# Kernel tuning notes

Hardware: AMD Instinct MI355X
Metric: run time of the kernel (lower is better)

Reference implementation:

```python
import jax, jax.numpy as jnp
import numpy as np

B, S, H, F, E, K = 4, 2048, 1024, 3584, 8, 2


def setup_inputs() -> dict:
    key = jax.random.key(0)
    ks = jax.random.split(key, 5)
    sc = 0.02
    return {
        "hidden_states": jax.random.normal(ks[0], (B, S, H), jnp.float32),
        "router_w": jax.random.normal(ks[1], (E, H), jnp.float32) * sc,
        "w1": jax.random.normal(ks[2], (E, F, H), jnp.float32) * sc,
        "v1": jax.random.normal(ks[3], (E, F, H), jnp.float32) * sc,
        "w2": jax.random.normal(ks[4], (E, F, H), jnp.float32) * sc,
    }


def reference(hidden_states, router_w, w1, v1, w2):
    b, s, h = hidden_states.shape
    x = hidden_states.reshape(-1, h)  # [T, H] tokens (transpose(0,1) is a no-op per-token)
    T = x.shape[0]
    n_exp = w1.shape[0]

    # --- Mixtral router: fp32 softmax, top-k, renormalize ---
    logits = x @ router_w.T  # [T, E]
    scores = jax.nn.softmax(logits.astype(jnp.float32), axis=-1)
    expert_weights, expert_indices = jax.lax.top_k(scores, K)  # [T, K]
    expert_weights = expert_weights / expert_weights.sum(axis=-1, keepdims=True)
    expert_weights = expert_weights.astype(x.dtype)

    # combine coefficients: coef[t, e] = sum_k weight[t,k] * (idx[t,k]==e)
    coef = jnp.zeros((T, n_exp), x.dtype)
    coef = coef.at[jnp.arange(T)[:, None], expert_indices].add(expert_weights)

    out = jnp.zeros_like(x)
    for e in range(n_exp):  # small fixed expert count
        hmid = jax.nn.silu(x @ w1[e].T) * (x @ v1[e].T)  # [T, F]
        out = out + coef[:, e:e + 1] * (hmid @ w2[e])  # [T, H]
    return out.reshape(b, s, h)
```

## Files before the change

### kernel.cpp

```cpp
#include <hip/hip_runtime.h>
#include <cstdint>
#include <cstddef>

#define T_TOK 8192
#define H_DIM 1024
#define F_DIM 3584
#define E_NUM 8
#define MAX_ROWS 17408
#define MAX_TILES 136

typedef __bf16 bf16_t;
typedef bf16_t bf16x8 __attribute__((ext_vector_type(8)));
typedef bf16_t bf16x4 __attribute__((ext_vector_type(4)));
typedef float floatx4 __attribute__((ext_vector_type(4)));

typedef const __attribute__((address_space(1))) void* gas_ptr;
typedef __attribute__((address_space(3))) void* las_ptr;

__device__ __forceinline__ void async_copy16(const void* g, void* l) {
    __builtin_amdgcn_global_load_lds((gas_ptr)g, (las_ptr)l, 16, 0, 0);
}

__global__ void cast_f32_to_bf16(const float* __restrict__ in, bf16_t* __restrict__ out, int n4) {
    int i = blockIdx.x * blockDim.x + threadIdx.x;
    if (i < n4) {
        const float4 v = ((const float4*)in)[i];
        bf16x4 o;
        o[0] = (bf16_t)v.x; o[1] = (bf16_t)v.y; o[2] = (bf16_t)v.z; o[3] = (bf16_t)v.w;
        ((bf16x4*)out)[i] = o;
    }
}

__global__ void transpose_cast_w2(const float* __restrict__ W2, bf16_t* __restrict__ W2T) {
    __shared__ bf16_t tile[32][34];
    const int e = blockIdx.z;
    const int f0 = blockIdx.x * 32;
    const int h0 = blockIdx.y * 32;
    const float* src = W2 + (size_t)e * F_DIM * H_DIM;
    bf16_t* dst = W2T + (size_t)e * H_DIM * F_DIM;
    const int tx = threadIdx.x;
    const int ty = threadIdx.y;
#pragma unroll
    for (int r = 0; r < 32; r += 8)
        tile[ty + r][tx] = (bf16_t)src[(size_t)(f0 + ty + r) * H_DIM + (h0 + tx)];
    __syncthreads();
#pragma unroll
    for (int r = 0; r < 32; r += 8)
        dst[(size_t)(h0 + ty + r) * F_DIM + (f0 + tx)] = tile[tx][ty + r];
}

__global__ void router_kernel(const float* __restrict__ X, const float* __restrict__ RW,
                              int* __restrict__ tok_e, float* __restrict__ tok_w) {
    const int lane = threadIdx.x & 63;
    const int wave = threadIdx.x >> 6;
    const int t = blockIdx.x * 4 + wave;
    const float* xp = X + (size_t)t * H_DIM;
    float xr[16];
#pragma unroll
    for (int j = 0; j < 16; ++j) xr[j] = xp[j * 64 + lane];
    float logits[E_NUM];
#pragma unroll
    for (int e = 0; e < E_NUM; ++e) {
        const float* rp = RW + e * H_DIM;
        float a = 0.f;
#pragma unroll
        for (int j = 0; j < 16; ++j) a += xr[j] * rp[j * 64 + lane];
#pragma unroll
        for (int s = 32; s; s >>= 1) a += __shfl_xor(a, s, 64);
        logits[e] = a;
    }
    if (lane == 0) {
        float mx = logits[0];
#pragma unroll
        for (int e = 1; e < E_NUM; ++e) mx = fmaxf(mx, logits[e]);
        float p[E_NUM], sum = 0.f;
#pragma unroll
        for (int e = 0; e < E_NUM; ++e) { p[e] = __expf(logits[e] - mx); sum += p[e]; }
#pragma unroll
        for (int e = 0; e < E_NUM; ++e) p[e] /= sum;
        int i0 = 0;
#pragma unroll
        for (int e = 1; e < E_NUM; ++e) if (p[e] > p[i0]) i0 = e;
        int i1 = (i0 == 0) ? 1 : 0;
#pragma unroll
        for (int e = 0; e < E_NUM; ++e) if (e != i0 && p[e] > p[i1]) i1 = e;
        const float s2 = p[i0] + p[i1];
        tok_e[t * 2 + 0] = i0; tok_w[t * 2 + 0] = p[i0] / s2;
        tok_e[t * 2 + 1] = i1; tok_w[t * 2 + 1] = p[i1] / s2;
    }
}

__global__ void build_assignments(const int* __restrict__ tok_e, const float* __restrict__ tok_w,
                                  int* __restrict__ asg_tok, float* __restrict__ asg_wt,
                                  int* __restrict__ tok_slot, int* __restrict__ tile_meta,
                                  int* __restrict__ n_tiles_out) {
    __shared__ int cnt[E_NUM];
    __shared__ int seg_start[E_NUM];
    __shared__ int seg_pad[E_NUM];
    const int tid = threadIdx.x;
    if (tid < E_NUM) cnt[tid] = 0;
    __syncthreads();
    for (int i = tid; i < T_TOK * 2; i += 1024) atomicAdd(&cnt[tok_e[i]], 1);
    __syncthreads();
    if (tid == 0) {
        int run = 0, nt = 0;
        for (int e = 0; e < E_NUM; ++e) {
            seg_start[e] = run;
            const int tiles = (cnt[e] + 127) >> 7;
            seg_pad[e] = tiles << 7;
            for (int j = 0; j < tiles; ++j) {
                tile_meta[nt * 2] = e;
                tile_meta[nt * 2 + 1] = run + j * 128;
                ++nt;
            }
            run += tiles << 7;
        }
        *n_tiles_out = nt;
    }
    __syncthreads();
    if (tid < E_NUM) cnt[tid] = 0;
    __syncthreads();
    for (int i = tid; i < T_TOK * 2; i += 1024) {
        const int e = tok_e[i];
        const int slot = atomicAdd(&cnt[e], 1);
        const int g = seg_start[e] + slot;
        asg_tok[g] = i >> 1;
        asg_wt[g] = tok_w[i];
        tok_slot[i] = g;
    }
    __syncthreads();
    for (int e = 0; e < E_NUM; ++e)
        for (int j = cnt[e] + tid; j < seg_pad[e]; j += 1024) {
            asg_tok[seg_start[e] + j] = -1;
            asg_wt[seg_start[e] + j] = 0.f;
        }
}


__global__ __launch_bounds__(256, 2)
void gemm1_glu(const bf16_t* __restrict__ X, const bf16_t* __restrict__ W1all,
               const bf16_t* __restrict__ V1all, const int* __restrict__ asg_tok,
               const float* __restrict__ asg_wt, const int* __restrict__ tile_meta,
               const int* __restrict__ n_tiles, bf16_t* __restrict__ Hmid) {
    const int tile = blockIdx.x;
    if (tile >= *n_tiles) return;
    const int e = tile_meta[tile * 2];
    const int row0 = tile_meta[tile * 2 + 1];
    const bf16_t* W1 = W1all + (size_t)e * F_DIM * H_DIM;
    const bf16_t* V1 = V1all + (size_t)e * F_DIM * H_DIM;

    __shared__ __attribute__((aligned(16))) bf16_t As[128 * 32];
    __shared__ __attribute__((aligned(16))) bf16_t B1s[128 * 32];
    __shared__ __attribute__((aligned(16))) bf16_t B2s[128 * 32];
    const int tid = threadIdx.x;
    const int lane = tid & 63;
    const int wave = tid >> 6;
    const int n0 = blockIdx.y * 128;
    const int wm = (wave >> 1) * 64;
    const int wn = (wave & 1) * 64;
    const int fr = lane & 15;
    const int q = lane >> 4;

    floatx4 acc1[4][4], acc2[4][4];
    const floatx4 zero = {0.f, 0.f, 0.f, 0.f};
#pragma unroll
    for (int a = 0; a < 4; ++a)
#pragma unroll
        for (int b = 0; b < 4; ++b) { acc1[a][b] = zero; acc2[a][b] = zero; }

    const int srow = tid >> 2;
    const int c = ((tid & 3) - ((tid >> 3) & 3)) & 3;
    const int scc = c * 8;
    const int ldsb0 = (tid & 192) * 16;
    const int ldsb1 = 4096 + ldsb0;

    int t0 = asg_tok[row0 + srow];      if (t0 < 0) t0 = 0;
    int t1 = asg_tok[row0 + 64 + srow]; if (t1 < 0) t1 = 0;
    const bf16_t* a0p = X + (size_t)t0 * H_DIM + scc;
    const bf16_t* a1p = X + (size_t)t1 * H_DIM + scc;
    const bf16_t* b1p0 = W1 + (size_t)(n0 + srow) * H_DIM + scc;
    const bf16_t* b1p1 = W1 + (size_t)(n0 + 64 + srow) * H_DIM + scc;
    const bf16_t* b2p0 = V1 + (size_t)(n0 + srow) * H_DIM + scc;
    const bf16_t* b2p1 = V1 + (size_t)(n0 + 64 + srow) * H_DIM + scc;

    for (int k0 = 0; k0 < H_DIM; k0 += 32) {
        async_copy16(a0p + k0, (char*)As + ldsb0);
        async_copy16(a1p + k0, (char*)As + ldsb1);
        async_copy16(b1p0 + k0, (char*)B1s + ldsb0);
        async_copy16(b1p1 + k0, (char*)B1s + ldsb1);
        async_copy16(b2p0 + k0, (char*)B2s + ldsb0);
        async_copy16(b2p1 + k0, (char*)B2s + ldsb1);
        __syncthreads();

        bf16x8 af[4], b1f[4], b2f[4];
#pragma unroll
        for (int mi = 0; mi < 4; ++mi) {
            const int r = wm + mi * 16 + fr;
            const int sl = (q + ((r >> 1) & 3)) & 3;
            af[mi] = *(const bf16x8*)&As[r * 32 + sl * 8];
        }
#pragma unroll
        for (int ni = 0; ni < 4; ++ni) {
            const int r = wn + ni * 16 + fr;
            const int sl = (q + ((r >> 1) & 3)) & 3;
            b1f[ni] = *(const bf16x8*)&B1s[r * 32 + sl * 8];
            b2f[ni] = *(const bf16x8*)&B2s[r * 32 + sl * 8];
        }
#pragma unroll
        for (int mi = 0; mi < 4; ++mi)
#pragma unroll
            for (int ni = 0; ni < 4; ++ni) {
                acc1[mi][ni] = __builtin_amdgcn_mfma_f32_16x16x32_bf16(af[mi], b1f[ni], acc1[mi][ni], 0, 0, 0);
                acc2[mi][ni] = __builtin_amdgcn_mfma_f32_16x16x32_bf16(af[mi], b2f[ni], acc2[mi][ni], 0, 0, 0);
            }
        __syncthreads();
    }

#pragma unroll
    for (int mi = 0; mi < 4; ++mi) {
#pragma unroll
        for (int r = 0; r < 4; ++r) {
            const int gr = row0 + wm + mi * 16 + q * 4 + r;
            const float wt = asg_wt[gr];
            bf16_t* hp = Hmid + (size_t)gr * F_DIM + n0 + wn + fr;
#pragma unroll
            for (int ni = 0; ni < 4; ++ni) {
                const float s1 = acc1[mi][ni][r];
                const float s2 = acc2[mi][ni][r];
                const float val = (s1 / (1.f + __expf(-s1))) * s2 * wt;
                hp[ni * 16] = (bf16_t)val;
            }
        }
    }
}

__global__ __launch_bounds__(256, 2)
void gemm2_out(const bf16_t* __restrict__ Hmid, const bf16_t* __restrict__ W2Tall,
               const int* __restrict__ tile_meta, const int* __restrict__ n_tiles,
               float* __restrict__ Oasm) {
    const int tile = blockIdx.x;
    if (tile >= *n_tiles) return;
    const int e = tile_meta[tile * 2];
    const int row0 = tile_meta[tile * 2 + 1];
    const bf16_t* W2T = W2Tall + (size_t)e * H_DIM * F_DIM;

    __shared__ __attribute__((aligned(16))) bf16_t As[128 * 32];
    __shared__ __attribute__((aligned(16))) bf16_t Bs[128 * 32];
    const int tid = threadIdx.x;
    const int lane = tid & 63;
    const int wave = tid >> 6;
    const int n0 = blockIdx.y * 128;
    const int wm = (wave >> 1) * 64;
    const int wn = (wave & 1) * 64;
    const int fr = lane & 15;
    const int q = lane >> 4;

    floatx4 acc[4][4];
    const floatx4 zero = {0.f, 0.f, 0.f, 0.f};
#pragma unroll
    for (int a = 0; a < 4; ++a)
#pragma unroll
        for (int b = 0; b < 4; ++b) acc[a][b] = zero;

    const int srow = tid >> 2;
    const int c = ((tid & 3) - ((tid >> 3) & 3)) & 3;
    const int scc = c * 8;
    const int ldsb0 = (tid & 192) * 16;
    const int ldsb1 = 4096 + ldsb0;

    const bf16_t* a0p = Hmid + (size_t)(row0 + srow) * F_DIM + scc;
    const bf16_t* a1p = Hmid + (size_t)(row0 + 64 + srow) * F_DIM + scc;
    const bf16_t* b0p = W2T + (size_t)(n0 + srow) * F_DIM + scc;
    const bf16_t* b1p = W2T + (size_t)(n0 + 64 + srow) * F_DIM + scc;

    for (int k0 = 0; k0 < F_DIM; k0 += 32) {
        async_copy16(a0p + k0, (char*)As + ldsb0);
        async_copy16(a1p + k0, (char*)As + ldsb1);
        async_copy16(b0p + k0, (char*)Bs + ldsb0);
        async_copy16(b1p + k0, (char*)Bs + ldsb1);
        __syncthreads();

        bf16x8 af[4], bf[4];
#pragma unroll
        for (int mi = 0; mi < 4; ++mi) {
            const int r = wm + mi * 16 + fr;
            const int sl = (q + ((r >> 1) & 3)) & 3;
            af[mi] = *(const bf16x8*)&As[r * 32 + sl * 8];
        }
#pragma unroll
        for (int ni = 0; ni < 4; ++ni) {
            const int r = wn + ni * 16 + fr;
            const int sl = (q + ((r >> 1) & 3)) & 3;
            bf[ni] = *(const bf16x8*)&Bs[r * 32 + sl * 8];
        }
#pragma unroll
        for (int mi = 0; mi < 4; ++mi)
#pragma unroll
            for (int ni = 0; ni < 4; ++ni)
                acc[mi][ni] = __builtin_amdgcn_mfma_f32_16x16x32_bf16(af[mi], bf[ni], acc[mi][ni], 0, 0, 0);
        __syncthreads();
    }

#pragma unroll
    for (int mi = 0; mi < 4; ++mi) {
#pragma unroll
        for (int r = 0; r < 4; ++r) {
            const int gr = row0 + wm + mi * 16 + q * 4 + r;
            float* op = Oasm + (size_t)gr * H_DIM + n0 + wn + fr;
#pragma unroll
            for (int ni = 0; ni < 4; ++ni)
                op[ni * 16] = acc[mi][ni][r];
        }
    }
}

__global__ void combine_kernel(const float* __restrict__ Oasm, const int* __restrict__ tok_slot,
                               float* __restrict__ Out) {
    const int t = blockIdx.x;
    const int s0 = tok_slot[t * 2];
    const int s1 = tok_slot[t * 2 + 1];
    const float4 v0 = ((const float4*)(Oasm + (size_t)s0 * H_DIM))[threadIdx.x];
    const float4 v1 = ((const float4*)(Oasm + (size_t)s1 * H_DIM))[threadIdx.x];
    float4 o; o.x = v0.x + v1.x; o.y = v0.y + v1.y; o.z = v0.z + v1.z; o.w = v0.w + v1.w;
    ((float4*)(Out + (size_t)t * H_DIM))[threadIdx.x] = o;
}

extern "C" void kernel_launch(void* const* d_in, const int* in_sizes, int n_in,
                              void* d_out, int out_size, void* d_ws, size_t ws_size,
                              hipStream_t stream) {
    const float* x  = (const float*)d_in[0];
    const float* rw = (const float*)d_in[1];
    const float* w1 = (const float*)d_in[2];
    const float* v1 = (const float*)d_in[3];
    const float* w2 = (const float*)d_in[4];
    float* out = (float*)d_out;

    char* ws = (char*)d_ws;
    const size_t MB = 1024 * 1024;
    bf16_t* xb   = (bf16_t*)(ws + 0);
    bf16_t* w1b  = (bf16_t*)(ws + 16 * MB);
    bf16_t* v1b  = (bf16_t*)(ws + 72 * MB);
    bf16_t* hmid = (bf16_t*)(ws + 128 * MB);
    bf16_t* w2t  = (bf16_t*)(ws + 0);
    float*  oasm = (float*)(ws + 56 * MB);
    char* meta = ws + 128 * MB + (size_t)MAX_ROWS * F_DIM * 2;
    int*   asg_tok  = (int*)meta;                meta += MAX_ROWS * 4;
    float* asg_wt   = (float*)meta;              meta += MAX_ROWS * 4;
    int*   tok_slot = (int*)meta;                meta += T_TOK * 2 * 4;
    int*   tok_e    = (int*)meta;                meta += T_TOK * 2 * 4;
    float* tok_w    = (float*)meta;              meta += T_TOK * 2 * 4;
    int*   tile_meta = (int*)meta;               meta += MAX_TILES * 2 * 4;
    int*   n_tiles   = (int*)meta;               meta += 4;

    const int nx4 = T_TOK * H_DIM / 4;
    const int nw4 = E_NUM * F_DIM * H_DIM / 4;
    cast_f32_to_bf16<<<nx4 / 256, 256, 0, stream>>>(x, xb, nx4);
    cast_f32_to_bf16<<<nw4 / 256, 256, 0, stream>>>(w1, w1b, nw4);
    cast_f32_to_bf16<<<nw4 / 256, 256, 0, stream>>>(v1, v1b, nw4);
    router_kernel<<<T_TOK / 4, 256, 0, stream>>>(x, rw, tok_e, tok_w);
    build_assignments<<<1, 1024, 0, stream>>>(tok_e, tok_w, asg_tok, asg_wt,
                                              tok_slot, tile_meta, n_tiles);
    gemm1_glu<<<dim3(MAX_TILES, F_DIM / 128), 256, 0, stream>>>(
        xb, w1b, v1b, asg_tok, asg_wt, tile_meta, n_tiles, hmid);
    transpose_cast_w2<<<dim3(F_DIM / 32, H_DIM / 32, E_NUM), dim3(32, 8), 0, stream>>>(w2, w2t);
    gemm2_out<<<dim3(MAX_TILES, H_DIM / 128), 256, 0, stream>>>(
        hmid, w2t, tile_meta, n_tiles, oasm);
    combine_kernel<<<T_TOK, 256, 0, stream>>>(oasm, tok_slot, out);
}
```

Measured before the change: 926.5 us.

## Fuse x cast into router, parallelize assignment build, widen GEMM K-tile

The router kernel now also writes the bf16 copy of the activations, which removes the separate activation cast launch. The single-block assignment builder is replaced by a histogram, a scan and a ballot-based scatter kernel, so routing bookkeeping is spread across many blocks while keeping a deterministic slot order. Both expert GEMMs now stage K=64 per iteration with an XOR-swizzled LDS layout, halving the number of barriers, and their launch-bounds occupancy hints are raised. The larger LDS tiles and higher occupancy targets may cause register spills or limit residency.

```diff
diff --git a/kernel.cpp b/kernel.cpp
--- a/kernel.cpp
+++ b/kernel.cpp
@@ -6,6 +6,8 @@
 #define H_DIM 1024
 #define F_DIM 3584
 #define E_NUM 8
+#define NASG (T_TOK * 2)
+#define NBLK 64
 #define MAX_ROWS 17408
 #define MAX_TILES 136
 
@@ -50,7 +52,8 @@
 }
 
 __global__ void router_kernel(const float* __restrict__ X, const float* __restrict__ RW,
-                              int* __restrict__ tok_e, float* __restrict__ tok_w) {
+                              int* __restrict__ tok_e, float* __restrict__ tok_w,
+                              bf16_t* __restrict__ xb) {
     const int lane = threadIdx.x & 63;
     const int wave = threadIdx.x >> 6;
     const int t = blockIdx.x * 4 + wave;
@@ -58,6 +61,9 @@
     float xr[16];
 #pragma unroll
     for (int j = 0; j < 16; ++j) xr[j] = xp[j * 64 + lane];
+    bf16_t* xo = xb + (size_t)t * H_DIM;
+#pragma unroll
+    for (int j = 0; j < 16; ++j) xo[j * 64 + lane] = (bf16_t)xr[j];
     float logits[E_NUM];
 #pragma unroll
     for (int e = 0; e < E_NUM; ++e) {
@@ -90,54 +96,74 @@
     }
 }
 
-__global__ void build_assignments(const int* __restrict__ tok_e, const float* __restrict__ tok_w,
-                                  int* __restrict__ asg_tok, float* __restrict__ asg_wt,
-                                  int* __restrict__ tok_slot, int* __restrict__ tile_meta,
-                                  int* __restrict__ n_tiles_out) {
-    __shared__ int cnt[E_NUM];
-    __shared__ int seg_start[E_NUM];
-    __shared__ int seg_pad[E_NUM];
+__global__ void hist_kernel(const int* __restrict__ tok_e, int* __restrict__ blk_cnt) {
+    __shared__ int h[E_NUM];
     const int tid = threadIdx.x;
-    if (tid < E_NUM) cnt[tid] = 0;
+    if (tid < E_NUM) h[tid] = 0;
     __syncthreads();
-    for (int i = tid; i < T_TOK * 2; i += 1024) atomicAdd(&cnt[tok_e[i]], 1);
+    atomicAdd(&h[tok_e[blockIdx.x * 256 + tid]], 1);
     __syncthreads();
-    if (tid == 0) {
+    if (tid < E_NUM) blk_cnt[blockIdx.x * E_NUM + tid] = h[tid];
+}
+
+__global__ void scan_kernel(const int* __restrict__ blk_cnt, int* __restrict__ boff,
+                            int* __restrict__ tile_meta, int* __restrict__ n_tiles,
+                            int* __restrict__ asg_tok, float* __restrict__ asg_wt) {
+    __shared__ int s_start[E_NUM], s_cnt[E_NUM], s_pad[E_NUM];
+    if (threadIdx.x == 0) {
         int run = 0, nt = 0;
         for (int e = 0; e < E_NUM; ++e) {
-            seg_start[e] = run;
-            const int tiles = (cnt[e] + 127) >> 7;
-            seg_pad[e] = tiles << 7;
+            int c = 0;
+            for (int b = 0; b < NBLK; ++b) c += blk_cnt[b * E_NUM + e];
+            const int tiles = (c + 127) >> 7;
+            s_start[e] = run; s_cnt[e] = c; s_pad[e] = tiles << 7;
             for (int j = 0; j < tiles; ++j) {
                 tile_meta[nt * 2] = e;
                 tile_meta[nt * 2 + 1] = run + j * 128;
                 ++nt;
             }
+            int r = run;
+            for (int b = 0; b < NBLK; ++b) { boff[b * E_NUM + e] = r; r += blk_cnt[b * E_NUM + e]; }
             run += tiles << 7;
         }
-        *n_tiles_out = nt;
-    }
-    __syncthreads();
-    if (tid < E_NUM) cnt[tid] = 0;
-    __syncthreads();
-    for (int i = tid; i < T_TOK * 2; i += 1024) {
-        const int e = tok_e[i];
-        const int slot = atomicAdd(&cnt[e], 1);
-        const int g = seg_start[e] + slot;
-        asg_tok[g] = i >> 1;
-        asg_wt[g] = tok_w[i];
-        tok_slot[i] = g;
+        *n_tiles = nt;
     }
     __syncthreads();
     for (int e = 0; e < E_NUM; ++e)
-        for (int j = cnt[e] + tid; j < seg_pad[e]; j += 1024) {
-            asg_tok[seg_start[e] + j] = -1;
-            asg_wt[seg_start[e] + j] = 0.f;
-        }
-}
-
-
-__global__ __launch_bounds__(256, 2)
+        for (int j = s_cnt[e] + threadIdx.x; j < s_pad[e]; j += 256) {
+            asg_tok[s_start[e] + j] = -1;
+            asg_wt[s_start[e] + j] = 0.f;
+        }
+}
+
+__global__ void scatter_kernel(const int* __restrict__ tok_e, const float* __restrict__ tok_w,
+                               const int* __restrict__ boff, int* __restrict__ asg_tok,
+                               float* __restrict__ asg_wt, int* __restrict__ tok_slot) {
+    __shared__ int wcnt[4][E_NUM];
+    const int tid = threadIdx.x;
+    const int lane = tid & 63;
+    const int w = tid >> 6;
+    const int i = blockIdx.x * 256 + tid;
+    const int e = tok_e[i];
+    const unsigned long long lt = (1ULL << lane) - 1ULL;
+    int myrank = 0;
+#pragma unroll
+    for (int eq = 0; eq < E_NUM; ++eq) {
+        const unsigned long long m = __ballot(e == eq);
+        if (e == eq) myrank = __popcll(m & lt);
+        if (lane == 0) wcnt[w][eq] = __popcll(m);
+    }
+    __syncthreads();
+    int base = 0;
+    for (int w2 = 0; w2 < w; ++w2) base += wcnt[w2][e];
+    const int g = boff[blockIdx.x * E_NUM + e] + base + myrank;
+    asg_tok[g] = i >> 1;
+    asg_wt[g] = tok_w[i];
+    tok_slot[i] = g;
+}
+
+
+__global__ __launch_bounds__(256, 3)
 void gemm1_glu(const bf16_t* __restrict__ X, const bf16_t* __restrict__ W1all,
                const bf16_t* __restrict__ V1all, const int* __restrict__ asg_tok,
                const float* __restrict__ asg_wt, const int* __restrict__ tile_meta,
@@ -149,9 +175,9 @@
     const bf16_t* W1 = W1all + (size_t)e * F_DIM * H_DIM;
     const bf16_t* V1 = V1all + (size_t)e * F_DIM * H_DIM;
 
-    __shared__ __attribute__((aligned(16))) bf16_t As[128 * 32];
-    __shared__ __attribute__((aligned(16))) bf16_t B1s[128 * 32];
-    __shared__ __attribute__((aligned(16))) bf16_t B2s[128 * 32];
+    __shared__ __attribute__((aligned(16))) bf16_t As[128 * 64];
+    __shared__ __attribute__((aligned(16))) bf16_t B1s[128 * 64];
+    __shared__ __attribute__((aligned(16))) bf16_t B2s[128 * 64];
     const int tid = threadIdx.x;
     const int lane = tid & 63;
     const int wave = tid >> 6;
@@ -168,51 +194,54 @@
 #pragma unroll
         for (int b = 0; b < 4; ++b) { acc1[a][b] = zero; acc2[a][b] = zero; }
 
-    const int srow = tid >> 2;
-    const int c = ((tid & 3) - ((tid >> 3) & 3)) & 3;
-    const int scc = c * 8;
-    const int ldsb0 = (tid & 192) * 16;
-    const int ldsb1 = 4096 + ldsb0;
-
-    int t0 = asg_tok[row0 + srow];      if (t0 < 0) t0 = 0;
-    int t1 = asg_tok[row0 + 64 + srow]; if (t1 < 0) t1 = 0;
-    const bf16_t* a0p = X + (size_t)t0 * H_DIM + scc;
-    const bf16_t* a1p = X + (size_t)t1 * H_DIM + scc;
-    const bf16_t* b1p0 = W1 + (size_t)(n0 + srow) * H_DIM + scc;
-    const bf16_t* b1p1 = W1 + (size_t)(n0 + 64 + srow) * H_DIM + scc;
-    const bf16_t* b2p0 = V1 + (size_t)(n0 + srow) * H_DIM + scc;
-    const bf16_t* b2p1 = V1 + (size_t)(n0 + 64 + srow) * H_DIM + scc;
-
-    for (int k0 = 0; k0 < H_DIM; k0 += 32) {
-        async_copy16(a0p + k0, (char*)As + ldsb0);
-        async_copy16(a1p + k0, (char*)As + ldsb1);
-        async_copy16(b1p0 + k0, (char*)B1s + ldsb0);
-        async_copy16(b1p1 + k0, (char*)B1s + ldsb1);
-        async_copy16(b2p0 + k0, (char*)B2s + ldsb0);
-        async_copy16(b2p1 + k0, (char*)B2s + ldsb1);
+    const int srow_lo = tid >> 3;
+    const int ch = (tid & 7) ^ (srow_lo & 7);
+    const int scc = ch * 8;
+    const int ldsb = wave * 1024;
+
+    const bf16_t* ap[4]; const bf16_t* b1p[4]; const bf16_t* b2p[4];
+#pragma unroll
+    for (int i = 0; i < 4; ++i) {
+        const int r = i * 32 + srow_lo;
+        int t = asg_tok[row0 + r]; if (t < 0) t = 0;
+        ap[i]  = X  + (size_t)t * H_DIM + scc;
+        b1p[i] = W1 + (size_t)(n0 + r) * H_DIM + scc;
+        b2p[i] = V1 + (size_t)(n0 + r) * H_DIM + scc;
+    }
+
+    for (int k0 = 0; k0 < H_DIM; k0 += 64) {
+#pragma unroll
+        for (int i = 0; i < 4; ++i) async_copy16(ap[i] + k0,  (char*)As  + i * 4096 + ldsb);
+#pragma unroll
+        for (int i = 0; i < 4; ++i) async_copy16(b1p[i] + k0, (char*)B1s + i * 4096 + ldsb);
+#pragma unroll
+        for (int i = 0; i < 4; ++i) async_copy16(b2p[i] + k0, (char*)B2s + i * 4096 + ldsb);
         __syncthreads();
 
-        bf16x8 af[4], b1f[4], b2f[4];
-#pragma unroll
-        for (int mi = 0; mi < 4; ++mi) {
-            const int r = wm + mi * 16 + fr;
-            const int sl = (q + ((r >> 1) & 3)) & 3;
-            af[mi] = *(const bf16x8*)&As[r * 32 + sl * 8];
-        }
-#pragma unroll
-        for (int ni = 0; ni < 4; ++ni) {
-            const int r = wn + ni * 16 + fr;
-            const int sl = (q + ((r >> 1) & 3)) & 3;
-            b1f[ni] = *(const bf16x8*)&B1s[r * 32 + sl * 8];
-            b2f[ni] = *(const bf16x8*)&B2s[r * 32 + sl * 8];
-        }
-#pragma unroll
-        for (int mi = 0; mi < 4; ++mi)
+#pragma unroll
+        for (int ks = 0; ks < 2; ++ks) {
+            bf16x8 af[4], b1f[4], b2f[4];
+#pragma unroll
+            for (int mi = 0; mi < 4; ++mi) {
+                const int r = wm + mi * 16 + fr;
+                const int sl = (ks * 4 + q) ^ (fr & 7);
+                af[mi] = *(const bf16x8*)&As[r * 64 + sl * 8];
+            }
 #pragma unroll
             for (int ni = 0; ni < 4; ++ni) {
-                acc1[mi][ni] = __builtin_amdgcn_mfma_f32_16x16x32_bf16(af[mi], b1f[ni], acc1[mi][ni], 0, 0, 0);
-                acc2[mi][ni] = __builtin_amdgcn_mfma_f32_16x16x32_bf16(af[mi], b2f[ni], acc2[mi][ni], 0, 0, 0);
-            }
+                const int r = wn + ni * 16 + fr;
+                const int sl = (ks * 4 + q) ^ (fr & 7);
+                b1f[ni] = *(const bf16x8*)&B1s[r * 64 + sl * 8];
+                b2f[ni] = *(const bf16x8*)&B2s[r * 64 + sl * 8];
+            }
+#pragma unroll
+            for (int mi = 0; mi < 4; ++mi)
+#pragma unroll
+                for (int ni = 0; ni < 4; ++ni) {
+                    acc1[mi][ni] = __builtin_amdgcn_mfma_f32_16x16x32_bf16(af[mi], b1f[ni], acc1[mi][ni], 0, 0, 0);
+                    acc2[mi][ni] = __builtin_amdgcn_mfma_f32_16x16x32_bf16(af[mi], b2f[ni], acc2[mi][ni], 0, 0, 0);
+                }
+        }
         __syncthreads();
     }
 
@@ -234,7 +263,7 @@
     }
 }
 
-__global__ __launch_bounds__(256, 2)
+__global__ __launch_bounds__(256, 4)
 void gemm2_out(const bf16_t* __restrict__ Hmid, const bf16_t* __restrict__ W2Tall,
                const int* __restrict__ tile_meta, const int* __restrict__ n_tiles,
                float* __restrict__ Oasm) {
@@ -244,8 +273,8 @@
     const int row0 = tile_meta[tile * 2 + 1];
     const bf16_t* W2T = W2Tall + (size_t)e * H_DIM * F_DIM;
 
-    __shared__ __attribute__((aligned(16))) bf16_t As[128 * 32];
-    __shared__ __attribute__((aligned(16))) bf16_t Bs[128 * 32];
+    __shared__ __attribute__((aligned(16))) bf16_t As[128 * 64];
+    __shared__ __attribute__((aligned(16))) bf16_t Bs[128 * 64];
     const int tid = threadIdx.x;
     const int lane = tid & 63;
     const int wave = tid >> 6;
@@ -262,42 +291,47 @@
 #pragma unroll
         for (int b = 0; b < 4; ++b) acc[a][b] = zero;
 
-    const int srow = tid >> 2;
-    const int c = ((tid & 3) - ((tid >> 3) & 3)) & 3;
-    const int scc = c * 8;
-    const int ldsb0 = (tid & 192) * 16;
-    const int ldsb1 = 4096 + ldsb0;
-
-    const bf16_t* a0p = Hmid + (size_t)(row0 + srow) * F_DIM + scc;
-    const bf16_t* a1p = Hmid + (size_t)(row0 + 64 + srow) * F_DIM + scc;
-    const bf16_t* b0p = W2T + (size_t)(n0 + srow) * F_DIM + scc;
-    const bf16_t* b1p = W2T + (size_t)(n0 + 64 + srow) * F_DIM + scc;
-
-    for (int k0 = 0; k0 < F_DIM; k0 += 32) {
-        async_copy16(a0p + k0, (char*)As + ldsb0);
-        async_copy16(a1p + k0, (char*)As + ldsb1);
-        async_copy16(b0p + k0, (char*)Bs + ldsb0);
-        async_copy16(b1p + k0, (char*)Bs + ldsb1);
+    const int srow_lo = tid >> 3;
+    const int ch = (tid & 7) ^ (srow_lo & 7);
+    const int scc = ch * 8;
+    const int ldsb = wave * 1024;
+
+    const bf16_t* ap[4]; const bf16_t* bp[4];
+#pragma unroll
+    for (int i = 0; i < 4; ++i) {
+        const int r = i * 32 + srow_lo;
+        ap[i] = Hmid + (size_t)(row0 + r) * F_DIM + scc;
+        bp[i] = W2T  + (size_t)(n0 + r) * F_DIM + scc;
+    }
+
+    for (int k0 = 0; k0 < F_DIM; k0 += 64) {
+#pragma unroll
+        for (int i = 0; i < 4; ++i) async_copy16(ap[i] + k0, (char*)As + i * 4096 + ldsb);
+#pragma unroll
+        for (int i = 0; i < 4; ++i) async_copy16(bp[i] + k0, (char*)Bs + i * 4096 + ldsb);
         __syncthreads();
 
-        bf16x8 af[4], bf[4];
-#pragma unroll
-        for (int mi = 0; mi < 4; ++mi) {
-            const int r = wm + mi * 16 + fr;
-            const int sl = (q + ((r >> 1) & 3)) & 3;
-            af[mi] = *(const bf16x8*)&As[r * 32 + sl * 8];
-        }
-#pragma unroll
-        for (int ni = 0; ni < 4; ++ni) {
-            const int r = wn + ni * 16 + fr;
-            const int sl = (q + ((r >> 1) & 3)) & 3;
-            bf[ni] = *(const bf16x8*)&Bs[r * 32 + sl * 8];
-        }
-#pragma unroll
-        for (int mi = 0; mi < 4; ++mi)
-#pragma unroll
-            for (int ni = 0; ni < 4; ++ni)
-                acc[mi][ni] = __builtin_amdgcn_mfma_f32_16x16x32_bf16(af[mi], bf[ni], acc[mi][ni], 0, 0, 0);
+#pragma unroll
+        for (int ks = 0; ks < 2; ++ks) {
+            bf16x8 af[4], bf[4];
+#pragma unroll
+            for (int mi = 0; mi < 4; ++mi) {
+                const int r = wm + mi * 16 + fr;
+                const int sl = (ks * 4 + q) ^ (fr & 7);
+                af[mi] = *(const bf16x8*)&As[r * 64 + sl * 8];
+            }
+#pragma unroll
+            for (int ni = 0; ni < 4; ++ni) {
+                const int r = wn + ni * 16 + fr;
+                const int sl = (ks * 4 + q) ^ (fr & 7);
+                bf[ni] = *(const bf16x8*)&Bs[r * 64 + sl * 8];
+            }
+#pragma unroll
+            for (int mi = 0; mi < 4; ++mi)
+#pragma unroll
+                for (int ni = 0; ni < 4; ++ni)
+                    acc[mi][ni] = __builtin_amdgcn_mfma_f32_16x16x32_bf16(af[mi], bf[ni], acc[mi][ni], 0, 0, 0);
+        }
         __syncthreads();
     }
 
@@ -346,20 +380,21 @@
     char* meta = ws + 128 * MB + (size_t)MAX_ROWS * F_DIM * 2;
     int*   asg_tok  = (int*)meta;                meta += MAX_ROWS * 4;
     float* asg_wt   = (float*)meta;              meta += MAX_ROWS * 4;
-    int*   tok_slot = (int*)meta;                meta += T_TOK * 2 * 4;
-    int*   tok_e    = (int*)meta;                meta += T_TOK * 2 * 4;
-    float* tok_w    = (float*)meta;              meta += T_TOK * 2 * 4;
+    int*   tok_slot = (int*)meta;                meta += NASG * 4;
+    int*   tok_e    = (int*)meta;                meta += NASG * 4;
+    float* tok_w    = (float*)meta;              meta += NASG * 4;
     int*   tile_meta = (int*)meta;               meta += MAX_TILES * 2 * 4;
-    int*   n_tiles   = (int*)meta;               meta += 4;
-
-    const int nx4 = T_TOK * H_DIM / 4;
+    int*   n_tiles   = (int*)meta;               meta += 16;
+    int*   blk_cnt   = (int*)meta;               meta += NBLK * E_NUM * 4;
+    int*   boff      = (int*)meta;               meta += NBLK * E_NUM * 4;
+
     const int nw4 = E_NUM * F_DIM * H_DIM / 4;
-    cast_f32_to_bf16<<<nx4 / 256, 256, 0, stream>>>(x, xb, nx4);
     cast_f32_to_bf16<<<nw4 / 256, 256, 0, stream>>>(w1, w1b, nw4);
     cast_f32_to_bf16<<<nw4 / 256, 256, 0, stream>>>(v1, v1b, nw4);
-    router_kernel<<<T_TOK / 4, 256, 0, stream>>>(x, rw, tok_e, tok_w);
-    build_assignments<<<1, 1024, 0, stream>>>(tok_e, tok_w, asg_tok, asg_wt,
-                                              tok_slot, tile_meta, n_tiles);
+    router_kernel<<<T_TOK / 4, 256, 0, stream>>>(x, rw, tok_e, tok_w, xb);
+    hist_kernel<<<NBLK, 256, 0, stream>>>(tok_e, blk_cnt);
+    scan_kernel<<<1, 256, 0, stream>>>(blk_cnt, boff, tile_meta, n_tiles, asg_tok, asg_wt);
+    scatter_kernel<<<NBLK, 256, 0, stream>>>(tok_e, tok_w, boff, asg_tok, asg_wt, tok_slot);
     gemm1_glu<<<dim3(MAX_TILES, F_DIM / 128), 256, 0, stream>>>(
         xb, w1b, v1b, asg_tok, asg_wt, tile_meta, n_tiles, hmid);
     transpose_cast_w2<<<dim3(F_DIM / 32, H_DIM / 32, E_NUM), dim3(32, 8), 0, stream>>>(w2, w2t);
```

New measurement: 1.593 ms. 1.72x slower.
